# Optimization experiments

Hardware: AMD Instinct MI355X
Metric: run time of the kernel (lower is better)

Reference implementation:

```python
import jax, jax.numpy as jnp
import numpy as np

B, S, D, H = 2, 2048, 2048, 16
HD = D // H  # 128


def setup_inputs() -> dict:
    key = jax.random.key(0)
    ks = jax.random.split(key, 7)
    x = jax.random.normal(ks[0], (B, S, D), jnp.float32)
    # 4 tree-position components per token (e.g. depth/branch coordinates)
    pos = jax.random.uniform(ks[1], (B, S, 4), jnp.float32, 0.0, 64.0)
    # tree/causal additive mask: 0 where attending is allowed, -1e9 otherwise
    causal = jnp.where(jnp.tril(jnp.ones((S, S), bool)), 0.0, -1e9).astype(jnp.float32)
    mask = jnp.broadcast_to(causal, (B, S, S))
    scale = D ** -0.5
    wq = jax.random.normal(ks[2], (D, D), jnp.float32) * scale
    wk = jax.random.normal(ks[3], (D, D), jnp.float32) * scale
    wv = jax.random.normal(ks[4], (D, D), jnp.float32) * scale
    wo = jax.random.normal(ks[5], (D, D), jnp.float32) * scale
    return {"x": x, "pos": pos, "mask": mask, "wq": wq, "wk": wk, "wv": wv, "wo": wo}


def reference(x, pos, mask, wq, wk, wv, wo):
    b, s, d = x.shape
    hd = HD
    # theta_of_dims: 1/10000^(arange(0,hd,8)[:hd//8]/hd) -> [hd//8]
    theta = 1.0 / (10000.0 ** (jnp.arange(0, hd, 8)[: hd // 8].astype(jnp.float32) / hd))
    q = (x @ wq.T).reshape(b, s, H, hd)
    k = (x @ wk.T).reshape(b, s, H, hd)
    v = (x @ wv.T).reshape(b, s, H, hd)
    # freqs: [b, s, hd//8, 4] flattened to [b, s, 1, hd//2]
    freqs = jnp.einsum('bij,k->bikj', pos, theta).reshape(b, s, 1, hd // 2)
    cos, sin = jnp.cos(freqs), jnp.sin(freqs)

    def rope(t):
        tr, ti = t[..., 0::2], t[..., 1::2]  # complex pairs (even=real, odd=imag)
        out_r = tr * cos - ti * sin
        out_i = tr * sin + ti * cos
        return jnp.stack([out_r, out_i], axis=-1).reshape(t.shape)

    q, k = rope(q), rope(k)
    scores = jnp.einsum('bqhd,bkhd->bhqk', q, k) / np.float32(np.sqrt(hd))
    scores = scores + mask[:, None, :, :]
    attn = jax.nn.softmax(scores, axis=-1)
    out = jnp.einsum('bhqk,bkhd->bqhd', attn, v).reshape(b, s, d)
    return out @ wo.T
```

## Files before the change

### kernel.cpp

```cpp
#include <hip/hip_runtime.h>
#include <cstdint>
#include <type_traits>

typedef __attribute__((ext_vector_type(8))) short short8;
typedef __attribute__((ext_vector_type(4))) float floatx4;

#define NB 2
#define NS 2048
#define ND 2048
#define NH 16
#define NHD 128

__device__ __forceinline__ float b2f(short s) {
  unsigned u = ((unsigned)(unsigned short)s) << 16;
  return __builtin_bit_cast(float, u);
}
__device__ __forceinline__ short f2b(float f) {
  unsigned u = __builtin_bit_cast(unsigned, f);
  unsigned r = (u + 0x7fffu + ((u >> 16) & 1u)) >> 16;
  return (short)(unsigned short)r;
}

__global__ void cast_all(const float* __restrict__ x, const float* __restrict__ wq,
                         const float* __restrict__ wk, const float* __restrict__ wv,
                         const float* __restrict__ wo, short* __restrict__ dst) {
  const int i = blockIdx.x * blockDim.x + threadIdx.x;
  const float* src;
  int off;
  if (i < 2097152) { src = x;  off = i; }
  else if (i < 3145728) { src = wq; off = i - 2097152; }
  else if (i < 4194304) { src = wk; off = i - 3145728; }
  else if (i < 5242880) { src = wv; off = i - 4194304; }
  else { src = wo; off = i - 5242880; }
  float4 v = ((const float4*)src)[off];
  short4 o;
  o.x = f2b(v.x); o.y = f2b(v.y); o.z = f2b(v.z); o.w = f2b(v.w);
  ((short4*)dst)[i] = o;
}

__device__ __forceinline__ void gld_lds16(const void* g, void* l) {
  __builtin_amdgcn_global_load_lds((const __attribute__((address_space(1))) void*)g,
                                   (__attribute__((address_space(3))) void*)l,
                                   16, 0, 0);
}

__global__ __launch_bounds__(256) void qkv_gemm(const short* __restrict__ A,
                                                const short* __restrict__ Bt,
                                                short* __restrict__ Qh,
                                                short* __restrict__ Kh,
                                                short* __restrict__ vlin) {
  constexpr int K = 2048;
  __shared__ short As[128 * 64];
  __shared__ short Bs[128 * 64];
  const int m0 = blockIdx.y * 128, n0 = blockIdx.x * 128;
  const int which = n0 >> 11;
  const int nl0 = n0 & 2047;
  const int t = threadIdx.x;
  const int wave = t >> 6, lane = t & 63, l15 = lane & 15, quad = lane >> 4;
  const int wm = (wave >> 1) * 64, wn = (wave & 1) * 64;

  floatx4 acc[4][4] = {};

  const int srow = t >> 3;
  const int scol = (t & 7) ^ (srow & 7);
  const short* Ag = A + (long)(m0 + srow) * K + scol * 8;
  const short* Bg = Bt + (long)(n0 + srow) * K + scol * 8;
  char* AsB = (char*)As;
  char* BsB = (char*)Bs;
  const int ldsOff = wave * 1024;

  for (int kt = 0; kt < K; kt += 64) {
#pragma unroll
    for (int i = 0; i < 4; ++i) {
      gld_lds16(Ag + kt + (long)(32 * i) * K, AsB + ldsOff + i * 4096);
      gld_lds16(Bg + kt + (long)(32 * i) * K, BsB + ldsOff + i * 4096);
    }
    __syncthreads();

#pragma unroll
    for (int half = 0; half < 2; ++half) {
      short8 a[4], b[4];
#pragma unroll
      for (int mi = 0; mi < 4; ++mi) {
        const int rr = wm + mi * 16 + l15;
        a[mi] = *(const short8*)&As[rr * 64 + (((half << 2) | quad) ^ (rr & 7)) * 8];
      }
#pragma unroll
      for (int ni = 0; ni < 4; ++ni) {
        const int rr = wn + ni * 16 + l15;
        b[ni] = *(const short8*)&Bs[rr * 64 + (((half << 2) | quad) ^ (rr & 7)) * 8];
      }
#pragma unroll
      for (int mi = 0; mi < 4; ++mi)
#pragma unroll
        for (int ni = 0; ni < 4; ++ni)
          acc[mi][ni] = __builtin_amdgcn_mfma_f32_16x16x32_bf16(a[mi], b[ni], acc[mi][ni], 0, 0, 0);
    }
    __syncthreads();
  }

  short* headDst = (which == 0) ? Qh : Kh;
#pragma unroll
  for (int mi = 0; mi < 4; ++mi) {
#pragma unroll
    for (int ni = 0; ni < 4; ++ni) {
#pragma unroll
      for (int r = 0; r < 4; ++r) {
        const int row = m0 + wm + mi * 16 + quad * 4 + r;
        const int col = nl0 + wn + ni * 16 + l15;
        const short v = f2b(acc[mi][ni][r]);
        if (which == 2) {
          vlin[(long)row * 2048 + col] = v;
        } else {
          const int bb = row >> 11, s = row & 2047, h = col >> 7, hd = col & 127;
          headDst[(((long)(bb * 16 + h) * 2048) + s) * 128 + hd] = v;
        }
      }
    }
  }
}

__global__ __launch_bounds__(256) void gemm_out(const short* __restrict__ A,
                                                const short* __restrict__ Bt,
                                                float* __restrict__ Cout) {
  constexpr int K = 2048, N = 2048;
  __shared__ short As[128 * 64];
  __shared__ short Bs[128 * 64];
  const int m0 = blockIdx.y * 128, n0 = blockIdx.x * 128;
  const int t = threadIdx.x;
  const int wave = t >> 6, lane = t & 63, l15 = lane & 15, quad = lane >> 4;
  const int wm = (wave >> 1) * 64, wn = (wave & 1) * 64;

  floatx4 acc[4][4] = {};

  const int srow = t >> 3;
  const int scol = (t & 7) ^ (srow & 7);
  const short* Ag = A + (long)(m0 + srow) * K + scol * 8;
  const short* Bg = Bt + (long)(n0 + srow) * K + scol * 8;
  char* AsB = (char*)As;
  char* BsB = (char*)Bs;
  const int ldsOff = wave * 1024;

  for (int kt = 0; kt < K; kt += 64) {
#pragma unroll
    for (int i = 0; i < 4; ++i) {
      gld_lds16(Ag + kt + (long)(32 * i) * K, AsB + ldsOff + i * 4096);
      gld_lds16(Bg + kt + (long)(32 * i) * K, BsB + ldsOff + i * 4096);
    }
    __syncthreads();

#pragma unroll
    for (int half = 0; half < 2; ++half) {
      short8 a[4], b[4];
#pragma unroll
      for (int mi = 0; mi < 4; ++mi) {
        const int rr = wm + mi * 16 + l15;
        a[mi] = *(const short8*)&As[rr * 64 + (((half << 2) | quad) ^ (rr & 7)) * 8];
      }
#pragma unroll
      for (int ni = 0; ni < 4; ++ni) {
        const int rr = wn + ni * 16 + l15;
        b[ni] = *(const short8*)&Bs[rr * 64 + (((half << 2) | quad) ^ (rr & 7)) * 8];
      }
#pragma unroll
      for (int mi = 0; mi < 4; ++mi)
#pragma unroll
        for (int ni = 0; ni < 4; ++ni)
          acc[mi][ni] = __builtin_amdgcn_mfma_f32_16x16x32_bf16(a[mi], b[ni], acc[mi][ni], 0, 0, 0);
    }
    __syncthreads();
  }

#pragma unroll
  for (int mi = 0; mi < 4; ++mi)
#pragma unroll
    for (int ni = 0; ni < 4; ++ni)
#pragma unroll
      for (int r = 0; r < 4; ++r) {
        const int row = m0 + wm + mi * 16 + quad * 4 + r;
        const int col = n0 + wn + ni * 16 + l15;
        Cout[(long)row * N + col] = acc[mi][ni][r];
      }
}

__global__ __launch_bounds__(256) void rope_vtrans(short* __restrict__ Qh,
                                                   short* __restrict__ Kh,
                                                   const float* __restrict__ pos,
                                                   const short* __restrict__ v_lin,
                                                   short* __restrict__ Vt) {
  __shared__ short tile[64 * 72];
  const int bx = blockIdx.x;
  if (bx < 4096) {
    const int tid = bx * 256 + threadIdx.x;
    const int kk = tid & 15;
    const int h = (tid >> 4) & 15;
    const int token = tid >> 8;
    const int bb = token >> 11, s = token & 2047;
    const float4 p4 = ((const float4*)pos)[token];
    const float pv[4] = {p4.x, p4.y, p4.z, p4.w};
    const float theta = exp2f(-(float)kk * 0.8304820237218406f);
    const long base = (((long)(bb * 16 + h)) * 2048 + s) * 128 + kk * 8;
    short8 q8 = *(short8*)(Qh + base);
    short8 k8 = *(short8*)(Kh + base);
    short8 qo, ko;
#pragma unroll
    for (int jj = 0; jj < 4; ++jj) {
      const float fr = pv[jj] * theta;
      float sn, c;
      __sincosf(fr, &sn, &c);
      {
        const float tr = b2f(q8[2 * jj]), ti = b2f(q8[2 * jj + 1]);
        qo[2 * jj] = f2b(tr * c - ti * sn);
        qo[2 * jj + 1] = f2b(tr * sn + ti * c);
      }
      {
        const float tr = b2f(k8[2 * jj]), ti = b2f(k8[2 * jj + 1]);
        ko[2 * jj] = f2b(tr * c - ti * sn);
        ko[2 * jj + 1] = f2b(tr * sn + ti * c);
      }
    }
    *(short8*)(Qh + base) = qo;
    *(short8*)(Kh + base) = ko;
  } else {
    const int b2 = bx - 4096;
    const int s0 = (b2 & 31) * 64;
    const int hd0 = ((b2 >> 5) & 1) * 64;
    const int bh = b2 >> 6;
    const int bb = bh >> 4, h = bh & 15;
    const int t = threadIdx.x;
#pragma unroll
    for (int i = 0; i < 2; ++i) {
      const int ch = t + i * 256;
      const int r = ch >> 3, c = ch & 7;
      *(short8*)&tile[r * 72 + c * 8] =
          *(const short8*)(v_lin + (long)(bb * 2048 + s0 + r) * 2048 + h * 128 + hd0 + c * 8);
    }
    __syncthreads();
#pragma unroll
    for (int i = 0; i < 2; ++i) {
      const int ch = t + i * 256;
      const int r2 = ch >> 3, c2 = ch & 7;
      short8 o;
#pragma unroll
      for (int u = 0; u < 8; ++u) o[u] = tile[(c2 * 8 + u) * 72 + r2];
      *(short8*)(Vt + ((long)(bh * 128 + hd0 + r2)) * 2048 + s0 + c2 * 8) = o;
    }
  }
}

__global__ __launch_bounds__(256, 2) void flash(const short* __restrict__ Qh,
                                                const short* __restrict__ Kh,
                                                const short* __restrict__ Vt,
                                                short* __restrict__ ao) {
  __shared__ short Ks[64 * 136];
  __shared__ short Vts[128 * 68];
  __shared__ short Ps[4 * 32 * 72];
  const int a = blockIdx.x;
  const int bh = blockIdx.y;
  const int t = threadIdx.x, wave = t >> 6, lane = t & 63, l15 = lane & 15, quad = lane >> 4;
  const int sqb[2] = {a * 64, (31 - a) * 64};
  const int lastkt0 = a, lastkt1 = 31 - a;

  const short* Qbase = Qh + (long)bh * 2048 * 128;
  short8 aq[2][4];
#pragma unroll
  for (int rb = 0; rb < 2; ++rb)
#pragma unroll
    for (int ks = 0; ks < 4; ++ks)
      aq[rb][ks] = *(const short8*)(Qbase + (long)(sqb[rb] + wave * 16 + l15) * 128 + ks * 32 + quad * 8);

  const short* KgBase = Kh + (long)bh * 2048 * 128;
  const short* VgBase = Vt + (long)bh * 128 * 2048;

  short8 kreg[4], vreg[4];
#pragma unroll
  for (int i = 0; i < 4; ++i) {
    const int ch = t + i * 256;
    kreg[i] = *(const short8*)(KgBase + (long)(ch >> 4) * 128 + (ch & 15) * 8);
    vreg[i] = *(const short8*)(VgBase + (long)(ch >> 3) * 2048 + (ch & 7) * 8);
  }

  float l_part[2][4] = {};
  floatx4 acc_o[2][8] = {};
  const float CEXP = 0.12751745f;

  for (int kt = 0; kt <= lastkt1; ++kt) {
    const int k0 = kt * 64;
    if (kt > 0) __syncthreads();

#pragma unroll
    for (int i = 0; i < 4; ++i) {
      const int ch = t + i * 256;
      *(short8*)&Ks[(ch >> 4) * 136 + (ch & 15) * 8] = kreg[i];
      *(short8*)&Vts[(ch >> 3) * 68 + (ch & 7) * 8] = vreg[i];
    }
    __syncthreads();

    if (kt < lastkt1) {
      const short* Kg = KgBase + (long)(k0 + 64) * 128;
      const short* Vg = VgBase + (k0 + 64);
#pragma unroll
      for (int i = 0; i < 4; ++i) {
        const int ch = t + i * 256;
        kreg[i] = *(const short8*)(Kg + (long)(ch >> 4) * 128 + (ch & 15) * 8);
        vreg[i] = *(const short8*)(Vg + (long)(ch >> 3) * 2048 + (ch & 7) * 8);
      }
    }

    const bool dgf[2] = {kt == lastkt0, kt == lastkt1};

    auto step = [&](auto DO0C) {
      constexpr bool DO0 = decltype(DO0C)::value;
      floatx4 accs[2][4] = {};
#pragma unroll
      for (int ks = 0; ks < 4; ++ks) {
#pragma unroll
        for (int ni = 0; ni < 4; ++ni) {
          const short8 bk = *(const short8*)&Ks[(ni * 16 + l15) * 136 + ks * 32 + quad * 8];
          accs[1][ni] = __builtin_amdgcn_mfma_f32_16x16x32_bf16(aq[1][ks], bk, accs[1][ni], 0, 0, 0);
          if (DO0)
            accs[0][ni] = __builtin_amdgcn_mfma_f32_16x16x32_bf16(aq[0][ks], bk, accs[0][ni], 0, 0, 0);
        }
      }
#pragma unroll
      for (int rb = 0; rb < 2; ++rb) {
        if (rb == 0 && !DO0) continue;
        const bool dg = dgf[rb];
#pragma unroll
        for (int r = 0; r < 4; ++r) {
          const int qrow = sqb[rb] + wave * 16 + quad * 4 + r;
#pragma unroll
          for (int ni = 0; ni < 4; ++ni) {
            float e = exp2f(accs[rb][ni][r] * CEXP);
            if (dg && (k0 + ni * 16 + l15) > qrow) e = 0.f;
            Ps[wave * 2304 + (rb * 16 + quad * 4 + r) * 72 + ni * 16 + l15] = f2b(e);
            l_part[rb][r] += e;
          }
        }
      }
#pragma unroll
      for (int ks2 = 0; ks2 < 2; ++ks2) {
        short8 ap1 = *(const short8*)&Ps[wave * 2304 + (16 + l15) * 72 + ks2 * 32 + quad * 8];
        short8 ap0;
        if (DO0) ap0 = *(const short8*)&Ps[wave * 2304 + l15 * 72 + ks2 * 32 + quad * 8];
#pragma unroll
        for (int nh = 0; nh < 8; ++nh) {
          const short8 bv = *(const short8*)&Vts[(nh * 16 + l15) * 68 + ks2 * 32 + quad * 8];
          acc_o[1][nh] = __builtin_amdgcn_mfma_f32_16x16x32_bf16(ap1, bv, acc_o[1][nh], 0, 0, 0);
          if (DO0)
            acc_o[0][nh] = __builtin_amdgcn_mfma_f32_16x16x32_bf16(ap0, bv, acc_o[0][nh], 0, 0, 0);
        }
      }
    };

    if (kt <= lastkt0)
      step(std::integral_constant<bool, true>{});
    else
      step(std::integral_constant<bool, false>{});
  }

  const int bb = bh >> 4, h = bh & 15;
#pragma unroll
  for (int rb = 0; rb < 2; ++rb) {
#pragma unroll
    for (int r = 0; r < 4; ++r) {
      float rs = l_part[rb][r];
#pragma unroll
      for (int mm = 8; mm >= 1; mm >>= 1) rs += __shfl_xor(rs, mm, 16);
      const float inv = 1.0f / rs;
      const int s = sqb[rb] + wave * 16 + quad * 4 + r;
      const long rowbase = ((long)(bb * 2048 + s)) * 2048 + h * 128;
#pragma unroll
      for (int nh = 0; nh < 8; ++nh) ao[rowbase + nh * 16 + l15] = f2b(acc_o[rb][nh][r] * inv);
    }
  }
}

extern "C" void kernel_launch(void* const* d_in, const int* in_sizes, int n_in,
                              void* d_out, int out_size, void* d_ws, size_t ws_size,
                              hipStream_t stream) {
  const float* x = (const float*)d_in[0];
  const float* pos = (const float*)d_in[1];
  const float* wq = (const float*)d_in[3];
  const float* wk = (const float*)d_in[4];
  const float* wv = (const float*)d_in[5];
  const float* wo = (const float*)d_in[6];
  float* out = (float*)d_out;

  char* ws = (char*)d_ws;
  const size_t MB = 1024 * 1024;
  short* xb    = (short*)(ws + 0);
  short* wqkvb = (short*)(ws + 16 * MB);
  short* wob   = (short*)(ws + 40 * MB);
  short* Qh    = (short*)(ws + 48 * MB);
  short* Kh    = (short*)(ws + 64 * MB);
  short* Vt    = (short*)(ws + 80 * MB);
  short* vlin  = (short*)(ws + 96 * MB);
  short* ao    = (short*)(ws + 96 * MB);

  cast_all<<<24576, 256, 0, stream>>>(x, wq, wk, wv, wo, xb);

  qkv_gemm<<<dim3(48, 32), 256, 0, stream>>>(xb, wqkvb, Qh, Kh, vlin);

  rope_vtrans<<<6144, 256, 0, stream>>>(Qh, Kh, pos, vlin, Vt);

  flash<<<dim3(16, 32), 256, 0, stream>>>(Qh, Kh, Vt, ao);

  gemm_out<<<dim3(16, 32), 256, 0, stream>>>(ao, wob, out);
}
```

Measured before the change: 414.4 us.

## Double-buffer K/V LDS tiles and replace padding with XOR swizzle in flash

The flash kernel now keeps two LDS buffers for K and V. The next tile is written into the alternate buffer after the current tile's compute, so each iteration needs one barrier instead of two. The padded row strides (136/68/72) are replaced with unpadded layouts that use XOR swizzling on 16-byte chunks to avoid LDS bank conflicts, applied to K, V^T and the P staging buffer. LDS use grows from about 52 KB to about 80 KB per block. With launch bounds requesting 2 blocks per CU this may be tight, and the added index arithmetic slightly raises ALU cost.

Result: slower. 458.4 us (+10.6%).

```diff
diff --git a/kernel.cpp b/kernel.cpp
--- a/kernel.cpp
+++ b/kernel.cpp
@@ -252,9 +252,9 @@
                                                 const short* __restrict__ Kh,
                                                 const short* __restrict__ Vt,
                                                 short* __restrict__ ao) {
-  __shared__ short Ks[64 * 136];
-  __shared__ short Vts[128 * 68];
-  __shared__ short Ps[4 * 32 * 72];
+  __shared__ short Ks[2][64 * 128];
+  __shared__ short Vts[2][128 * 64];
+  __shared__ short Ps[4][32 * 64];
   const int a = blockIdx.x;
   const int bh = blockIdx.y;
   const int t = threadIdx.x, wave = t >> 6, lane = t & 63, l15 = lane & 15, quad = lane >> 4;
@@ -279,22 +279,22 @@
     kreg[i] = *(const short8*)(KgBase + (long)(ch >> 4) * 128 + (ch & 15) * 8);
     vreg[i] = *(const short8*)(VgBase + (long)(ch >> 3) * 2048 + (ch & 7) * 8);
   }
+#pragma unroll
+  for (int i = 0; i < 4; ++i) {
+    const int ch = t + i * 256;
+    *(short8*)&Ks[0][(ch >> 4) * 128 + ((ch & 15) ^ ((ch >> 4) & 7)) * 8] = kreg[i];
+    *(short8*)&Vts[0][(ch >> 3) * 64 + ((ch & 7) ^ ((ch >> 3) & 7)) * 8] = vreg[i];
+  }
 
   float l_part[2][4] = {};
   floatx4 acc_o[2][8] = {};
   const float CEXP = 0.12751745f;
+  const int cxor = l15 & 7;
+  const int axor = (2 * (l15 >> 2)) & 7;
 
   for (int kt = 0; kt <= lastkt1; ++kt) {
     const int k0 = kt * 64;
-    if (kt > 0) __syncthreads();
-
-#pragma unroll
-    for (int i = 0; i < 4; ++i) {
-      const int ch = t + i * 256;
-      *(short8*)&Ks[(ch >> 4) * 136 + (ch & 15) * 8] = kreg[i];
-      *(short8*)&Vts[(ch >> 3) * 68 + (ch & 7) * 8] = vreg[i];
-    }
-    __syncthreads();
+    const int p = kt & 1;
 
     if (kt < lastkt1) {
       const short* Kg = KgBase + (long)(k0 + 64) * 128;
@@ -307,6 +307,8 @@
       }
     }
 
+    __syncthreads();
+
     const bool dgf[2] = {kt == lastkt0, kt == lastkt1};
 
     auto step = [&](auto DO0C) {
@@ -316,7 +318,8 @@
       for (int ks = 0; ks < 4; ++ks) {
 #pragma unroll
         for (int ni = 0; ni < 4; ++ni) {
-          const short8 bk = *(const short8*)&Ks[(ni * 16 + l15) * 136 + ks * 32 + quad * 8];
+          const short8 bk =
+              *(const short8*)&Ks[p][(ni * 16 + l15) * 128 + ((4 * ks + quad) ^ cxor) * 8];
           accs[1][ni] = __builtin_amdgcn_mfma_f32_16x16x32_bf16(aq[1][ks], bk, accs[1][ni], 0, 0, 0);
           if (DO0)
             accs[0][ni] = __builtin_amdgcn_mfma_f32_16x16x32_bf16(aq[0][ks], bk, accs[0][ni], 0, 0, 0);
@@ -333,19 +336,22 @@
           for (int ni = 0; ni < 4; ++ni) {
             float e = exp2f(accs[rb][ni][r] * CEXP);
             if (dg && (k0 + ni * 16 + l15) > qrow) e = 0.f;
-            Ps[wave * 2304 + (rb * 16 + quad * 4 + r) * 72 + ni * 16 + l15] = f2b(e);
+            Ps[wave][(rb * 16 + quad * 4 + r) * 64 +
+                     ((2 * ni + (l15 >> 3)) ^ (2 * quad)) * 8 + (l15 & 7)] = f2b(e);
             l_part[rb][r] += e;
           }
         }
       }
 #pragma unroll
       for (int ks2 = 0; ks2 < 2; ++ks2) {
-        short8 ap1 = *(const short8*)&Ps[wave * 2304 + (16 + l15) * 72 + ks2 * 32 + quad * 8];
+        const short8 ap1 =
+            *(const short8*)&Ps[wave][(16 + l15) * 64 + ((4 * ks2 + quad) ^ axor) * 8];
         short8 ap0;
-        if (DO0) ap0 = *(const short8*)&Ps[wave * 2304 + l15 * 72 + ks2 * 32 + quad * 8];
+        if (DO0) ap0 = *(const short8*)&Ps[wave][l15 * 64 + ((4 * ks2 + quad) ^ axor) * 8];
 #pragma unroll
         for (int nh = 0; nh < 8; ++nh) {
-          const short8 bv = *(const short8*)&Vts[(nh * 16 + l15) * 68 + ks2 * 32 + quad * 8];
+          const short8 bv =
+              *(const short8*)&Vts[p][(nh * 16 + l15) * 64 + ((4 * ks2 + quad) ^ cxor) * 8];
           acc_o[1][nh] = __builtin_amdgcn_mfma_f32_16x16x32_bf16(ap1, bv, acc_o[1][nh], 0, 0, 0);
           if (DO0)
             acc_o[0][nh] = __builtin_amdgcn_mfma_f32_16x16x32_bf16(ap0, bv, acc_o[0][nh], 0, 0, 0);
@@ -357,6 +363,16 @@
       step(std::integral_constant<bool, true>{});
     else
       step(std::integral_constant<bool, false>{});
+
+    if (kt < lastkt1) {
+      const int pn = p ^ 1;
+#pragma unroll
+      for (int i = 0; i < 4; ++i) {
+        const int ch = t + i * 256;
+        *(short8*)&Ks[pn][(ch >> 4) * 128 + ((ch & 15) ^ ((ch >> 4) & 7)) * 8] = kreg[i];
+        *(short8*)&Vts[pn][(ch >> 3) * 64 + ((ch & 7) ^ ((ch >> 3) & 7)) * 8] = vreg[i];
+      }
+    }
   }
 
   const int bb = bh >> 4, h = bh & 15;
```
